# Performance work log

Measured on AMD Instinct MI355X. Metric: run time of the kernel, lower is better.

## Reference

```python
import jax, jax.numpy as jnp
import numpy as np

T0 = 16
EPS = 1.1920929e-07  # torch fp32 finfo eps used by F.rms_norm default

def rmsnorm(v):
    return v * jax.lax.rsqrt(jnp.mean(v * v, axis=-1, keepdims=True) + EPS)

def apply_rotary_emb(x, cos, sin):
    # x: (B, S, H, C); rotate-half style as in source
    d = x.shape[-1] // 2
    x1, x2 = x[..., :d], x[..., d:]
    return jnp.concatenate([x1 * cos + x2 * sin, -x1 * sin + x2 * cos], axis=-1)

def setup_inputs():
    key = jax.random.key(0)
    ks = jax.random.split(key, 8)
    B, T, C, H = 8, 8192, 128, 8
    S = (T0 // 4) * T0 + 1  # 64 selected tokens + 1 sink = 65
    x = jax.random.normal(ks[0], (B, T, C), jnp.float32)
    # RoPE tables over the sink-augmented attention sequence, head_dim/2 = 64
    inv = 1.0 / (10000.0 ** (jnp.arange(C // 2, dtype=jnp.float32) / (C // 2)))
    ang = jnp.arange(S, dtype=jnp.float32)[:, None] * inv[None, :]
    cos = jnp.cos(ang)[None, :, None, :]  # (1, 65, 1, 64)
    sin = jnp.sin(ang)[None, :, None, :]
    sink = 0.02 * jax.random.normal(ks[1], (1, H, C), jnp.float32)
    W_qkvg = 0.02 * jax.random.normal(ks[2], (4 * C * H, C), jnp.float32)
    patch_w = 0.02 * jax.random.normal(ks[3], (T0 * C,), jnp.float32)
    W_out = 0.02 * jax.random.normal(ks[4], (C, H * C), jnp.float32)
    tao = jnp.array([1.2, 1.2], jnp.float32)
    return {"x": x, "cos": cos, "sin": sin, "sink": sink, "W_qkvg": W_qkvg,
            "patch_w": patch_w, "W_out": W_out, "tao": tao}

def reference(x, cos, sin, sink, W_qkvg, patch_w, W_out, tao):
    B, T, C = x.shape
    H = sink.shape[1]
    Np = T // T0  # T chosen as multiple of T0, so pad P = 0
    # --- patch scoring + topk patch selection (patch_toks) ---
    xp = x.reshape(B, Np, T0 * C)
    score = jax.nn.softmax(rmsnorm(xp) @ patch_w, axis=-1)  # (B, Np)
    _, I = jax.lax.top_k(score, T0 // 4)                    # top 4 patches
    I = jnp.sort(I, axis=-1)                                # (B, 4)
    # --- qkvg projection over ALL tokens, then patch-flattened chunk ---
    qkvg = x @ W_qkvg.T                                     # (B, T, 4*C*H)
    qkvg_p = qkvg.reshape(B, Np, 4 * T0 * C * H)
    n = T0 * C * H
    q_p = qkvg_p[..., 0 * n:1 * n]
    k_p = qkvg_p[..., 1 * n:2 * n]
    v_p = qkvg_p[..., 2 * n:3 * n]
    g_p = qkvg_p[..., 3 * n:4 * n]
    def gather(p):  # (B, Np, n) -> (B, 4*T0, H, C) via selected patches
        return jnp.take_along_axis(p, I[:, :, None], axis=1).reshape(B, -1, H, C)
    q, k, v, g = gather(q_p), gather(k_p), gather(v_p), gather(g_p)
    # --- sink token prepend ---
    s = jnp.broadcast_to(sink[:, None], (B, 1, H, C))
    q = jnp.concatenate([s, q], axis=1)  # (B, 65, H, C)
    k = jnp.concatenate([s, k], axis=1)
    v = jnp.concatenate([s, v], axis=1)
    # --- RoPE + RMSNorm + learned temperatures ---
    q = rmsnorm(apply_rotary_emb(q, cos, sin)) * tao[0]
    k = rmsnorm(apply_rotary_emb(k, cos, sin)) * tao[1]
    # --- causal SDPA (scale 1/sqrt(C)), drop sink row ---
    S = q.shape[1]
    att = jnp.einsum('bshc,bthc->bhst', q, k) / jnp.sqrt(jnp.float32(C))
    causal = jnp.tril(jnp.ones((S, S), dtype=bool))
    att = jax.nn.softmax(jnp.where(causal, att, -jnp.inf), axis=-1)
    y = jnp.einsum('bhst,bthc->bshc', att, v)[:, 1:]  # (B, 64, H, C)
    # --- sigmoid gating + output projection ---
    y = y * jax.nn.sigmoid(g)
    return y.reshape(B, y.shape[1], H * C) @ W_out.T  # (B, 64, C)
```

## Files before the change

### kernel.cpp

```cpp
#include <hip/hip_runtime.h>
#include <hip/hip_bf16.h>

#define EPSR 1.1920929e-07f

#define OFF_SCORE 0LL
#define OFF_WQT   8192LL
#define OFF_WO4   532480LL
#define OFF_SEL   663552LL
#define OFF_YG    4757504LL

__device__ __forceinline__ bool is_bf16_in(const void* tao) {
    unsigned int w = *(const unsigned int*)tao;
    return (w >> 16) == (w & 0xffffu);
}

__device__ __forceinline__ float ldin(const void* p, long long i, bool bf) {
    if (bf) return __uint_as_float(((unsigned int)(((const unsigned short*)p)[i])) << 16);
    return ((const float*)p)[i];
}

__device__ __forceinline__ float4 ldin4(const void* p, long long i, bool bf) {
    if (bf) {
        ushort4 u = ((const ushort4*)p)[i >> 2];
        return make_float4(__uint_as_float((unsigned int)u.x << 16),
                           __uint_as_float((unsigned int)u.y << 16),
                           __uint_as_float((unsigned int)u.z << 16),
                           __uint_as_float((unsigned int)u.w << 16));
    }
    return ((const float4*)p)[i >> 2];
}

__global__ __launch_bounds__(256) void k_prep_score(const void* Wq, const void* Wo,
                                                    const void* x, const void* pw,
                                                    const void* tao, float* ws) {
    bool bf = is_bf16_in(tao);
    __shared__ float tile[16448];
    int tid = threadIdx.x;
    if (blockIdx.x < 1024) {
        int lane = tid & 63, wid = tid >> 6;
        int patch = blockIdx.x * 4 + wid;
        long long base = (long long)patch * 2048;
        float ss = 0.f, dt = 0.f;
        #pragma unroll
        for (int i = 0; i < 8; i++) {
            int e = i * 256 + lane * 4;
            float4 v = ldin4(x, base + e, bf);
            float4 w = ldin4(pw, e, bf);
            ss += v.x * v.x + v.y * v.y + v.z * v.z + v.w * v.w;
            dt += v.x * w.x + v.y * w.y + v.z * w.z + v.w * w.w;
        }
        #pragma unroll
        for (int o = 32; o; o >>= 1) { ss += __shfl_xor(ss, o); dt += __shfl_xor(dt, o); }
        if (lane == 0) ws[OFF_SCORE + patch] = dt * rsqrtf(ss * (1.f / 2048.f) + EPSR);
    } else if (blockIdx.x < 1088) {
        float* WqT = ws + OFF_WQT;
        int j0 = (blockIdx.x - 1024) * 64;
        #pragma unroll
        for (int rep = 0; rep < 8; rep++) {
            int jr = rep * 8 + (tid >> 5);
            int c4 = (tid & 31) * 4;
            float4 v = ldin4(Wq, ((long long)(j0 + jr)) * 128 + c4, bf);
            float* t = &tile[jr * 129 + c4];
            t[0] = v.x; t[1] = v.y; t[2] = v.z; t[3] = v.w;
        }
        __syncthreads();
        #pragma unroll
        for (int rep = 0; rep < 8; rep++) {
            int c = rep * 16 + (tid >> 4);
            int jq = (tid & 15) * 4;
            float4 v = make_float4(tile[jq * 129 + c], tile[(jq + 1) * 129 + c],
                                   tile[(jq + 2) * 129 + c], tile[(jq + 3) * 129 + c]);
            *(float4*)&WqT[c * 4096 + j0 + jq] = v;
        }
    } else {
        float* Wo4 = ws + OFF_WO4;
        int co0 = (blockIdx.x - 1088) * 16;
        #pragma unroll
        for (int rep = 0; rep < 16; rep++) {
            float4 v = ldin4(Wo, ((long long)(co0 + rep)) * 1024 + tid * 4, bf);
            *(float4*)&tile[rep * 1028 + tid * 4] = v;
        }
        __syncthreads();
        #pragma unroll
        for (int rep = 0; rep < 16; rep++) {
            int idx = rep * 256 + tid;
            int fg = idx >> 4, co = idx & 15;
            float4 v = *(const float4*)&tile[co * 1028 + fg * 4];
            *(float4*)&Wo4[(fg * 128 + co0 + co) * 4] = v;
        }
    }
}

__global__ __launch_bounds__(256) void k_qkvg(const void* x, const void* cosp, const void* sinp,
                                              const void* tao, float* ws) {
    bool bf = is_bf16_in(tao);
    int blk = blockIdx.x;
    int jc = blk & 15, bp = blk >> 4;
    int b = bp >> 2, p = bp & 3;
    __shared__ float4 xs4[512];
    __shared__ int tok0s;
    int tid = threadIdx.x;
    if (tid < 64) {
        const float4* sp = (const float4*)(ws + OFF_SCORE + b * 512);
        float4 a = sp[tid * 2], c = sp[tid * 2 + 1];
        float v[8];
        v[0] = a.x; v[1] = a.y; v[2] = a.z; v[3] = a.w;
        v[4] = c.x; v[5] = c.y; v[6] = c.z; v[7] = c.w;
        int win[4];
        #pragma unroll
        for (int k = 0; k < 4; k++) {
            float bm = v[0]; int bi = 0;
            #pragma unroll
            for (int i = 1; i < 8; i++) if (v[i] > bm) { bm = v[i]; bi = i; }
            int gi = tid * 8 + bi;
            #pragma unroll
            for (int o = 32; o; o >>= 1) {
                float om = __shfl_xor(bm, o); int oi = __shfl_xor(gi, o);
                if (om > bm || (om == bm && oi < gi)) { bm = om; gi = oi; }
            }
            win[k] = gi;
            if ((gi >> 3) == tid) v[gi & 7] = -INFINITY;
        }
        if (tid == 0) {
            int a0 = win[0], a1 = win[1], a2 = win[2], a3 = win[3], tmp;
            if (a0 > a1) { tmp = a0; a0 = a1; a1 = tmp; }
            if (a2 > a3) { tmp = a2; a2 = a3; a3 = tmp; }
            if (a0 > a2) { tmp = a0; a0 = a2; a2 = tmp; }
            if (a1 > a3) { tmp = a1; a1 = a3; a3 = tmp; }
            if (a1 > a2) { tmp = a1; a1 = a2; a2 = tmp; }
            int sorted[4] = {a0, a1, a2, a3};
            tok0s = sorted[p] * 16;
        }
    }
    __syncthreads();
    int tok0 = tok0s;
    long long xbase = ((long long)(b * 8192 + tok0)) * 128;
    for (int i = tid; i < 512; i += 256)
        xs4[i] = ldin4(x, xbase + i * 4, bf);
    __syncthreads();
    int tg = tid >> 6, jx = tid & 63;
    const float4* WqT4 = (const float4*)(ws + OFF_WQT);
    int wcol = jc * 64 + jx;
    float4 acc[4];
    #pragma unroll
    for (int t = 0; t < 4; t++) acc[t] = make_float4(0.f, 0.f, 0.f, 0.f);
    float4 nw0 = WqT4[0 * 1024 + wcol];
    float4 nw1 = WqT4[1 * 1024 + wcol];
    float4 nw2 = WqT4[2 * 1024 + wcol];
    float4 nw3 = WqT4[3 * 1024 + wcol];
    for (int c4 = 0; c4 < 32; c4++) {
        float4 w0 = nw0, w1 = nw1, w2 = nw2, w3 = nw3;
        if (c4 < 31) {
            nw0 = WqT4[(c4 * 4 + 4) * 1024 + wcol];
            nw1 = WqT4[(c4 * 4 + 5) * 1024 + wcol];
            nw2 = WqT4[(c4 * 4 + 6) * 1024 + wcol];
            nw3 = WqT4[(c4 * 4 + 7) * 1024 + wcol];
        }
        #pragma unroll
        for (int t = 0; t < 4; t++) {
            float4 xv = xs4[(tg * 4 + t) * 32 + c4];
            acc[t].x += xv.x * w0.x + xv.y * w1.x + xv.z * w2.x + xv.w * w3.x;
            acc[t].y += xv.x * w0.y + xv.y * w1.y + xv.z * w2.y + xv.w * w3.y;
            acc[t].z += xv.x * w0.z + xv.y * w1.z + xv.z * w2.z + xv.w * w3.z;
            acc[t].w += xv.x * w0.w + xv.y * w1.w + xv.z * w2.w + xv.w * w3.w;
        }
    }
    if (tg < 2) {
        float taov = (tg == 0) ? ldin(tao, 0, bf) : ldin(tao, 1, bf);
        bool hi = (jx & 16) != 0;
        int cc4 = (jx & 15) * 4;
        int soff = jc >> 2;
        #pragma unroll
        for (int t = 0; t < 4; t++) {
            int s = p * 16 + t * 4 + soff + 1;
            float4 cs = ldin4(cosp, (long long)s * 64 + cc4, bf);
            float4 sn = ldin4(sinp, (long long)s * 64 + cc4, bf);
            float4 own = acc[t], prt;
            prt.x = __shfl_xor(own.x, 16);
            prt.y = __shfl_xor(own.y, 16);
            prt.z = __shfl_xor(own.z, 16);
            prt.w = __shfl_xor(own.w, 16);
            float4 r;
            if (!hi) {
                r.x = own.x * cs.x + prt.x * sn.x;
                r.y = own.y * cs.y + prt.y * sn.y;
                r.z = own.z * cs.z + prt.z * sn.z;
                r.w = own.w * cs.w + prt.w * sn.w;
            } else {
                r.x = own.x * cs.x - prt.x * sn.x;
                r.y = own.y * cs.y - prt.y * sn.y;
                r.z = own.z * cs.z - prt.z * sn.z;
                r.w = own.w * cs.w - prt.w * sn.w;
            }
            float ss = r.x * r.x + r.y * r.y + r.z * r.z + r.w * r.w;
            #pragma unroll
            for (int ofs = 16; ofs; ofs >>= 1) ss += __shfl_xor(ss, ofs);
            float sc = rsqrtf(ss * (1.f / 128.f) + EPSR) * taov;
            acc[t].x = r.x * sc; acc[t].y = r.y * sc;
            acc[t].z = r.z * sc; acc[t].w = r.w * sc;
        }
    }
    float4* sel4 = (float4*)(ws + OFF_SEL);
    #pragma unroll
    for (int t = 0; t < 4; t++)
        sel4[(bp * 16 + tg * 4 + t) * 1024 + wcol] = acc[t];
}

__global__ __launch_bounds__(512, 4) void k_fused(const void* sink, const void* tao, float* ws) {
    bool bf = is_bf16_in(tao);
    const float* sel = ws + OFF_SEL;
    const float4* sel4 = (const float4*)sel;
    float* yg = ws + OFF_YG;
    int blk = blockIdx.x;
    int b = blk >> 6, h = (blk >> 3) & 7, u = blk & 7;
    int tid = threadIdx.x, lane = tid & 63, wid = tid >> 6;
    __shared__ float qs[8 * 132];
    __shared__ float ks[65 * 132];
    __shared__ float att[8 * 68];
    __shared__ float sinkv[128];
    __shared__ float4 part[8][32];

    if (tid < 128) sinkv[tid] = ldin(sink, h * 128 + tid, bf);
    for (int idx = tid; idx < 64 * 32; idx += 512) {
        int row = (idx >> 5) + 1, c4 = idx & 31;
        int r = row - 1, pp = r >> 4, sl = r & 15;
        long long kb4 = (((long long)(b * 4 + pp) * 16 + 4 + (sl >> 2)) * 1024) + (sl & 3) * 256 + h * 32 + c4;
        *(float4*)&ks[row * 132 + c4 * 4] = sel4[kb4];
    }
    if (tid < 256) {
        int lr = tid >> 5, c4 = tid & 31;
        int r = (lr < 4) ? (u * 4 + lr) : ((15 - u) * 4 + (lr - 4));
        int pp = r >> 4, sl = r & 15;
        long long qb4 = (((long long)(b * 4 + pp) * 16 + (sl >> 2)) * 1024) + (sl & 3) * 256 + h * 32 + c4;
        *(float4*)&qs[lr * 132 + c4 * 4] = sel4[qb4];
    }
    if (tid >= 256 && tid < 288) {
        int l = tid - 256;
        float4 v = ldin4(sink, h * 128 + l * 4, bf);
        float ss = v.x * v.x + v.y * v.y + v.z * v.z + v.w * v.w;
        #pragma unroll
        for (int ofs = 16; ofs; ofs >>= 1) ss += __shfl_xor(ss, ofs);
        float sc = rsqrtf(ss * (1.f / 128.f) + EPSR) * ldin(tao, 1, bf);
        float* d = &ks[l * 4];
        d[0] = v.x * sc; d[1] = v.y * sc; d[2] = v.z * sc; d[3] = v.w * sc;
    }
    __syncthreads();

    if (tid < 132) {
        int sT = tid & 3, tT = tid >> 2;
        int lsp = sT * 2;
        int s0g = (lsp < 4) ? (u * 4 + 1 + lsp) : ((15 - u) * 4 + 1 + (lsp - 4));
        int t0 = tT * 2;
        if (t0 <= s0g + 1) {
            int t1 = (t0 + 1 > 64) ? 64 : t0 + 1;
            const float* q0 = &qs[lsp * 132];
            const float* q1 = &qs[(lsp + 1) * 132];
            const float* k0 = &ks[t0 * 132];
            const float* k1 = &ks[t1 * 132];
            float a00 = 0.f, a01 = 0.f, a10 = 0.f, a11 = 0.f;
            #pragma unroll 4
            for (int c = 0; c < 128; c += 4) {
                float4 qa = *(const float4*)(q0 + c);
                float4 qb = *(const float4*)(q1 + c);
                float4 ka = *(const float4*)(k0 + c);
                float4 kb = *(const float4*)(k1 + c);
                a00 += qa.x * ka.x + qa.y * ka.y + qa.z * ka.z + qa.w * ka.w;
                a01 += qa.x * kb.x + qa.y * kb.y + qa.z * kb.z + qa.w * kb.w;
                a10 += qb.x * ka.x + qb.y * ka.y + qb.z * ka.z + qb.w * ka.w;
                a11 += qb.x * kb.x + qb.y * kb.y + qb.z * kb.z + qb.w * kb.w;
            }
            const float scale = 0.08838834764831845f;
            if (t0 <= s0g)     att[lsp * 68 + t0] = a00 * scale;
            if (t0 + 1 <= s0g) att[lsp * 68 + t0 + 1] = a01 * scale;
            att[(lsp + 1) * 68 + t0] = a10 * scale;
            if (t0 + 1 <= s0g + 1) att[(lsp + 1) * 68 + t0 + 1] = a11 * scale;
        }
    }
    __syncthreads();

    {
        int ls = wid;
        int s = (ls < 4) ? (u * 4 + 1 + ls) : ((15 - u) * 4 + 1 + (ls - 4));
        float x1 = (lane <= s) ? __expf(att[ls * 68 + lane]) : 0.f;
        float x2 = (lane == 0 && s == 64) ? __expf(att[ls * 68 + 64]) : 0.f;
        float sum = x1 + x2;
        #pragma unroll
        for (int ofs = 32; ofs; ofs >>= 1) sum += __shfl_xor(sum, ofs);
        float inv = 1.f / sum;
        att[ls * 68 + lane] = x1 * inv;
        if (lane < 4) att[ls * 68 + 64 + lane] = (lane == 0) ? x2 * inv : 0.f;
    }
    __syncthreads();

    {
        int th = tid >> 8;
        int row = (tid >> 5) & 7, c0 = (tid & 31) * 4;
        int s = (row < 4) ? (u * 4 + 1 + row) : ((15 - u) * 4 + 1 + (row - 4));
        const float* ar = &att[row * 68];
        float4 acc = make_float4(0.f, 0.f, 0.f, 0.f);
        if (th == 0) {
            {
                float4 a = *(const float4*)ar;
                float4 v0 = *(const float4*)&sinkv[c0];
                acc.x += a.x * v0.x; acc.y += a.x * v0.y; acc.z += a.x * v0.z; acc.w += a.x * v0.w;
                #pragma unroll
                for (int j = 1; j < 4; j++) {
                    int r = j - 1;
                    long long vb = (((long long)(b * 4) * 16 + 8 + (r >> 2)) * 4096) + (r & 3) * 1024 + h * 128 + c0;
                    float4 vt = *(const float4*)&sel[vb];
                    float aj = (j == 1) ? a.y : (j == 2) ? a.z : a.w;
                    acc.x += aj * vt.x; acc.y += aj * vt.y; acc.z += aj * vt.z; acc.w += aj * vt.w;
                }
            }
            #pragma unroll
            for (int t4 = 4; t4 <= 28; t4 += 4) {
                float4 a = *(const float4*)(ar + t4);
                #pragma unroll
                for (int j = 0; j < 4; j++) {
                    int r = t4 + j - 1;
                    int pp = r >> 4, sl = r & 15;
                    long long vb = (((long long)(b * 4 + pp) * 16 + 8 + (sl >> 2)) * 4096) + (sl & 3) * 1024 + h * 128 + c0;
                    float4 vt = *(const float4*)&sel[vb];
                    float aj = (j == 0) ? a.x : (j == 1) ? a.y : (j == 2) ? a.z : a.w;
                    acc.x += aj * vt.x; acc.y += aj * vt.y; acc.z += aj * vt.z; acc.w += aj * vt.w;
                }
            }
        } else if (s >= 32) {
            #pragma unroll
            for (int t4 = 32; t4 <= 60; t4 += 4) {
                float4 a = *(const float4*)(ar + t4);
                #pragma unroll
                for (int j = 0; j < 4; j++) {
                    int r = t4 + j - 1;
                    int pp = r >> 4, sl = r & 15;
                    long long vb = (((long long)(b * 4 + pp) * 16 + 8 + (sl >> 2)) * 4096) + (sl & 3) * 1024 + h * 128 + c0;
                    float4 vt = *(const float4*)&sel[vb];
                    float aj = (j == 0) ? a.x : (j == 1) ? a.y : (j == 2) ? a.z : a.w;
                    acc.x += aj * vt.x; acc.y += aj * vt.y; acc.z += aj * vt.z; acc.w += aj * vt.w;
                }
            }
            {
                float a = ar[64];
                int r = 63;
                int pp = r >> 4, sl = r & 15;
                long long vb = (((long long)(b * 4 + pp) * 16 + 8 + (sl >> 2)) * 4096) + (sl & 3) * 1024 + h * 128 + c0;
                float4 vt = *(const float4*)&sel[vb];
                acc.x += a * vt.x; acc.y += a * vt.y; acc.z += a * vt.z; acc.w += a * vt.w;
            }
        }
        if (th == 1) part[row][tid & 31] = acc;
        __syncthreads();
        if (th == 0) {
            float4 pr = part[row][tid & 31];
            acc.x += pr.x; acc.y += pr.y; acc.z += pr.z; acc.w += pr.w;
            int rg = s - 1;
            int pp = rg >> 4, sl = rg & 15, tl = 12 + (sl >> 2);
            long long gb = (((long long)(b * 4 + pp) * 16 + tl) * 4096) + (sl & 3) * 1024 + h * 128 + c0;
            float4 g = *(const float4*)&sel[gb];
            acc.x /= (1.f + __expf(-g.x));
            acc.y /= (1.f + __expf(-g.y));
            acc.z /= (1.f + __expf(-g.z));
            acc.w /= (1.f + __expf(-g.w));
            long long yb = ((long long)(b * 64 + rg)) * 1024 + h * 128 + c0;
            *(float4*)&yg[yb] = acc;
        }
    }
}

__global__ __launch_bounds__(512) void k_out(const void* tao, float* ws, void* out) {
    bool bf = is_bf16_in(tao);
    int blk = blockIdx.x;
    int b = blk >> 5, rq = (blk >> 1) & 15, ch = blk & 1;
    int r0 = rq * 4, cbase = ch * 64;
    __shared__ float4 ylds[4 * 257];
    __shared__ float part[8][4][64];
    int tid = threadIdx.x;
    const float4* yg4 = (const float4*)(ws + OFF_YG);
    for (int i = tid; i < 1024; i += 512) {
        int row = i >> 8, f4 = i & 255;
        ylds[row * 257 + f4] = yg4[(b * 64 + r0 + row) * 256 + f4];
    }
    __syncthreads();
    int co4 = tid & 15, row = (tid >> 4) & 3, fs = tid >> 6;
    const float4* Wo44 = (const float4*)(ws + OFF_WO4);
    const float4* yrow = &ylds[row * 257];
    float a0 = 0.f, a1 = 0.f, a2 = 0.f, a3 = 0.f;
    int g0 = fs * 32;
    #pragma unroll 4
    for (int g = g0; g < g0 + 32; g++) {
        float4 y = yrow[g];
        const float4* wp = &Wo44[g * 128 + cbase + co4 * 4];
        float4 w0 = wp[0], w1 = wp[1], w2 = wp[2], w3 = wp[3];
        a0 += y.x * w0.x + y.y * w0.y + y.z * w0.z + y.w * w0.w;
        a1 += y.x * w1.x + y.y * w1.y + y.z * w1.z + y.w * w1.w;
        a2 += y.x * w2.x + y.y * w2.y + y.z * w2.z + y.w * w2.w;
        a3 += y.x * w3.x + y.y * w3.y + y.z * w3.z + y.w * w3.w;
    }
    part[fs][row][co4 * 4 + 0] = a0;
    part[fs][row][co4 * 4 + 1] = a1;
    part[fs][row][co4 * 4 + 2] = a2;
    part[fs][row][co4 * 4 + 3] = a3;
    __syncthreads();
    if (tid < 256) {
        int row2 = tid >> 6, co = tid & 63;
        float v = 0.f;
        #pragma unroll
        for (int f = 0; f < 8; f++) v += part[f][row2][co];
        long long oidx = ((long long)(b * 64 + r0 + row2)) * 128 + cbase + co;
        if (bf) ((__hip_bfloat16*)out)[oidx] = __float2bfloat16(v);
        else    ((float*)out)[oidx] = v;
    }
}

extern "C" void kernel_launch(void* const* d_in, const int* in_sizes, int n_in,
                              void* d_out, int out_size, void* d_ws, size_t ws_size,
                              hipStream_t stream) {
    const void* x    = d_in[0];
    const void* cosp = d_in[1];
    const void* sinp = d_in[2];
    const void* sink = d_in[3];
    const void* Wq   = d_in[4];
    const void* pw   = d_in[5];
    const void* Wo   = d_in[6];
    const void* tao  = d_in[7];
    float* ws = (float*)d_ws;

    k_prep_score<<<dim3(1096), dim3(256), 0, stream>>>(Wq, Wo, x, pw, tao, ws);
    k_qkvg <<<dim3(512), dim3(256), 0, stream>>>(x, cosp, sinp, tao, ws);
    k_fused<<<dim3(512), dim3(512), 0, stream>>>(sink, tao, ws);
    k_out  <<<dim3(256), dim3(512), 0, stream>>>(tao, ws, d_out);
}
```

Baseline: 139.5 us.

## Stage qkvg weight chunks and attention V rows in shared memory

The qkvg projection kernel now loads the transposed weight in 16-row chunks into LDS, with a sync around each chunk, instead of register-prefetching straight from global memory. The attention kernel copies all 64 V rows for its head into the shared buffer previously used for K, so the att·V loop reads LDS instead of scattered global loads. This aims to cut global-load latency and repeated address math. In exchange it adds more barriers and uses more LDS, which may lower occupancy. It also drops the register prefetch overlap in the projection.

```diff
diff --git a/kernel.cpp b/kernel.cpp
--- a/kernel.cpp
+++ b/kernel.cpp
@@ -98,6 +98,7 @@
     int jc = blk & 15, bp = blk >> 4;
     int b = bp >> 2, p = bp & 3;
     __shared__ float4 xs4[512];
+    __shared__ float4 wlds[1024];
     __shared__ int tok0s;
     int tid = threadIdx.x;
     if (tid < 64) {
@@ -137,32 +138,35 @@
     long long xbase = ((long long)(b * 8192 + tok0)) * 128;
     for (int i = tid; i < 512; i += 256)
         xs4[i] = ldin4(x, xbase + i * 4, bf);
-    __syncthreads();
     int tg = tid >> 6, jx = tid & 63;
     const float4* WqT4 = (const float4*)(ws + OFF_WQT);
     int wcol = jc * 64 + jx;
     float4 acc[4];
     #pragma unroll
     for (int t = 0; t < 4; t++) acc[t] = make_float4(0.f, 0.f, 0.f, 0.f);
-    float4 nw0 = WqT4[0 * 1024 + wcol];
-    float4 nw1 = WqT4[1 * 1024 + wcol];
-    float4 nw2 = WqT4[2 * 1024 + wcol];
-    float4 nw3 = WqT4[3 * 1024 + wcol];
-    for (int c4 = 0; c4 < 32; c4++) {
-        float4 w0 = nw0, w1 = nw1, w2 = nw2, w3 = nw3;
-        if (c4 < 31) {
-            nw0 = WqT4[(c4 * 4 + 4) * 1024 + wcol];
-            nw1 = WqT4[(c4 * 4 + 5) * 1024 + wcol];
-            nw2 = WqT4[(c4 * 4 + 6) * 1024 + wcol];
-            nw3 = WqT4[(c4 * 4 + 7) * 1024 + wcol];
-        }
-        #pragma unroll
-        for (int t = 0; t < 4; t++) {
-            float4 xv = xs4[(tg * 4 + t) * 32 + c4];
-            acc[t].x += xv.x * w0.x + xv.y * w1.x + xv.z * w2.x + xv.w * w3.x;
-            acc[t].y += xv.x * w0.y + xv.y * w1.y + xv.z * w2.y + xv.w * w3.y;
-            acc[t].z += xv.x * w0.z + xv.y * w1.z + xv.z * w2.z + xv.w * w3.z;
-            acc[t].w += xv.x * w0.w + xv.y * w1.w + xv.z * w2.w + xv.w * w3.w;
+    for (int chunk = 0; chunk < 8; chunk++) {
+        __syncthreads();
+        #pragma unroll
+        for (int r = 0; r < 4; r++) {
+            int crow = chunk * 16 + tg * 4 + r;
+            wlds[(tg * 4 + r) * 64 + jx] = WqT4[(long long)crow * 1024 + jc * 64 + jx];
+        }
+        __syncthreads();
+        #pragma unroll
+        for (int c4l = 0; c4l < 4; c4l++) {
+            int c4 = chunk * 4 + c4l;
+            float4 w0 = wlds[(c4l * 4 + 0) * 64 + jx];
+            float4 w1 = wlds[(c4l * 4 + 1) * 64 + jx];
+            float4 w2 = wlds[(c4l * 4 + 2) * 64 + jx];
+            float4 w3 = wlds[(c4l * 4 + 3) * 64 + jx];
+            #pragma unroll
+            for (int t = 0; t < 4; t++) {
+                float4 xv = xs4[(tg * 4 + t) * 32 + c4];
+                acc[t].x += xv.x * w0.x + xv.y * w1.x + xv.z * w2.x + xv.w * w3.x;
+                acc[t].y += xv.x * w0.y + xv.y * w1.y + xv.z * w2.y + xv.w * w3.y;
+                acc[t].z += xv.x * w0.z + xv.y * w1.z + xv.z * w2.z + xv.w * w3.z;
+                acc[t].w += xv.x * w0.w + xv.y * w1.w + xv.z * w2.w + xv.w * w3.w;
+            }
         }
     }
     if (tg < 2) {
@@ -290,6 +294,12 @@
         att[ls * 68 + lane] = x1 * inv;
         if (lane < 4) att[ls * 68 + 64 + lane] = (lane == 0) ? x2 * inv : 0.f;
     }
+    for (int idx = tid; idx < 64 * 32; idx += 512) {
+        int r = idx >> 5, c4 = idx & 31;
+        int pp = r >> 4, sl = r & 15;
+        long long vb4 = (((long long)(b * 4 + pp) * 16 + 8 + (sl >> 2)) * 1024) + (sl & 3) * 256 + h * 32 + c4;
+        *(float4*)&ks[r * 132 + c4 * 4] = sel4[vb4];
+    }
     __syncthreads();
 
     {
@@ -305,9 +315,7 @@
                 acc.x += a.x * v0.x; acc.y += a.x * v0.y; acc.z += a.x * v0.z; acc.w += a.x * v0.w;
                 #pragma unroll
                 for (int j = 1; j < 4; j++) {
-                    int r = j - 1;
-                    long long vb = (((long long)(b * 4) * 16 + 8 + (r >> 2)) * 4096) + (r & 3) * 1024 + h * 128 + c0;
-                    float4 vt = *(const float4*)&sel[vb];
+                    float4 vt = *(const float4*)&ks[(j - 1) * 132 + c0];
                     float aj = (j == 1) ? a.y : (j == 2) ? a.z : a.w;
                     acc.x += aj * vt.x; acc.y += aj * vt.y; acc.z += aj * vt.z; acc.w += aj * vt.w;
                 }
@@ -317,10 +325,7 @@
                 float4 a = *(const float4*)(ar + t4);
                 #pragma unroll
                 for (int j = 0; j < 4; j++) {
-                    int r = t4 + j - 1;
-                    int pp = r >> 4, sl = r & 15;
-                    long long vb = (((long long)(b * 4 + pp) * 16 + 8 + (sl >> 2)) * 4096) + (sl & 3) * 1024 + h * 128 + c0;
-                    float4 vt = *(const float4*)&sel[vb];
+                    float4 vt = *(const float4*)&ks[(t4 + j - 1) * 132 + c0];
                     float aj = (j == 0) ? a.x : (j == 1) ? a.y : (j == 2) ? a.z : a.w;
                     acc.x += aj * vt.x; acc.y += aj * vt.y; acc.z += aj * vt.z; acc.w += aj * vt.w;
                 }
@@ -331,20 +336,14 @@
                 float4 a = *(const float4*)(ar + t4);
                 #pragma unroll
                 for (int j = 0; j < 4; j++) {
-                    int r = t4 + j - 1;
-                    int pp = r >> 4, sl = r & 15;
-                    long long vb = (((long long)(b * 4 + pp) * 16 + 8 + (sl >> 2)) * 4096) + (sl & 3) * 1024 + h * 128 + c0;
-                    float4 vt = *(const float4*)&sel[vb];
+                    float4 vt = *(const float4*)&ks[(t4 + j - 1) * 132 + c0];
                     float aj = (j == 0) ? a.x : (j == 1) ? a.y : (j == 2) ? a.z : a.w;
                     acc.x += aj * vt.x; acc.y += aj * vt.y; acc.z += aj * vt.z; acc.w += aj * vt.w;
                 }
             }
             {
                 float a = ar[64];
-                int r = 63;
-                int pp = r >> 4, sl = r & 15;
-                long long vb = (((long long)(b * 4 + pp) * 16 + 8 + (sl >> 2)) * 4096) + (sl & 3) * 1024 + h * 128 + c0;
-                float4 vt = *(const float4*)&sel[vb];
+                float4 vt = *(const float4*)&ks[63 * 132 + c0];
                 acc.x += a * vt.x; acc.y += a * vt.y; acc.z += a * vt.z; acc.w += a * vt.w;
             }
         }
```

New measurement: 139.6 us. About the same (+0.0%).
